# Kernel optimization log

Hardware: AMD Instinct MI355X
Metric: run time of the kernel (lower is better)

The kernel has to match this reference:

```python
import jax, jax.numpy as jnp
import numpy as np

LAMBDA_ENERGY = 0.1   # CONFIG['lambda_energy']
EPS = 1e-6            # CONFIG['eps']
TEMP = 1.0


def setup_inputs() -> dict:
    key = jax.random.key(0)
    k0, k1, k2, k3, k4 = jax.random.split(key, 5)
    B, S, D, N = 8, 4096, 512, 1024
    z_real = jax.random.normal(k0, (B, S, D), dtype=jnp.float32)
    z_imag = jax.random.normal(k1, (B, S, D), dtype=jnp.float32)
    # prev symbol distribution: a proper simplex distribution over symbols
    prev_sym_dist = jax.nn.softmax(jax.random.normal(k2, (B, S, N), dtype=jnp.float32), axis=-1)
    codebook = jax.random.normal(k3, (N, 2 * D), dtype=jnp.float32) * 0.2
    adjacency_energy = jax.random.normal(k4, (N, N), dtype=jnp.float32)
    return {"z_real": z_real, "z_imag": z_imag, "prev_sym_dist": prev_sym_dist,
            "codebook": codebook, "adjacency_energy": adjacency_energy}


def reference(z_real, z_imag, prev_sym_dist, codebook, adjacency_energy):
    D = z_real.shape[-1]
    z_flat = jnp.concatenate([z_real, z_imag], axis=-1)  # [B,S,2D]

    # squared-distance to codebook entries, normalized by feature dim
    d_content = (jnp.sum(z_flat * z_flat, axis=-1, keepdims=True)
                 + jnp.sum(codebook * codebook, axis=-1)
                 - 2.0 * jnp.einsum('bsd,nd->bsn', z_flat, codebook)) / z_flat.shape[-1]

    # ComplexityModulator (eval mode): running_var buffer == 1.0
    mag = jnp.sqrt(z_real * z_real + z_imag * z_imag)  # |z|
    batch_var = jnp.var(mag, ddof=1)                   # torch .var() is unbiased
    modulation = jax.nn.softplus(batch_var / (1.0 + EPS))

    # graph-bias gating
    graph_bias = jnp.einsum('bsn,nm->bsm', prev_sym_dist, adjacency_energy)
    d_total = d_content - (LAMBDA_ENERGY * modulation) * jax.nn.sigmoid(graph_bias)

    # eval path: soft_one_hot = softmax(logits / temp)
    probs = jax.nn.softmax(-d_total / TEMP, axis=-1)   # [B,S,N]
    z_q_flat = jnp.einsum('bsn,nd->bsd', probs, codebook)  # [B,S,2D]

    energy = jnp.mean(d_total)
    return z_q_flat[..., :D], z_q_flat[..., D:], energy
```

## Files before the change

### kernel.cpp

```cpp
#include <hip/hip_runtime.h>

typedef float    floatx4 __attribute__((ext_vector_type(4)));
typedef short    short8  __attribute__((ext_vector_type(8)));
typedef _Float16 h4      __attribute__((ext_vector_type(4)));

#define NROWS 32768
#define KD    1024
#define DD    512

__device__ __forceinline__ unsigned pk_bf16(unsigned hi_bits, unsigned lo_bits) {
    return __builtin_amdgcn_perm(hi_bits, lo_bits, 0x07060302u);
}

__device__ __forceinline__ void gload_lds16(const void* g, void* l) {
    __builtin_amdgcn_global_load_lds((__attribute__((address_space(1))) void*)(void*)g,
                                     (__attribute__((address_space(3))) void*)l,
                                     16, 0, 0);
}

__global__ void k_row(const float* __restrict__ zr, const float* __restrict__ zi,
                      unsigned short* __restrict__ zb,
                      float* __restrict__ zz, float* __restrict__ mgp) {
    int r = blockIdx.x, t = threadIdx.x;
    const float2* a2 = (const float2*)(zr + (size_t)r * DD);
    const float2* b2 = (const float2*)(zi + (size_t)r * DD);
    float2 a = a2[t], b = b2[t];
    unsigned* zrow = (unsigned*)(zb + (size_t)r * KD);
    zrow[t]       = pk_bf16(__float_as_uint(a.y), __float_as_uint(a.x));
    zrow[256 + t] = pk_bf16(__float_as_uint(b.y), __float_as_uint(b.x));
    float m0 = a.x * a.x + b.x * b.x;
    float m1 = a.y * a.y + b.y * b.y;
    float sm2 = m0 + m1;
    float smg = sqrtf(m0) + sqrtf(m1);
    for (int o = 32; o > 0; o >>= 1) { sm2 += __shfl_down(sm2, o); smg += __shfl_down(smg, o); }
    __shared__ float r2[4], rg[4];
    int wv = t >> 6, ln = t & 63;
    if (ln == 0) { r2[wv] = sm2; rg[wv] = smg; }
    __syncthreads();
    if (t == 0) {
        zz[r]  = r2[0] + r2[1] + r2[2] + r2[3];
        mgp[r] = rg[0] + rg[1] + rg[2] + rg[3];
    }
}

__global__ void k_prev(const float* __restrict__ p, unsigned short* __restrict__ pb) {
    size_t i = ((size_t)blockIdx.x * 256 + threadIdx.x) * 8;
    const uint4* g = (const uint4*)(p + i);
    uint4 u0 = g[0], u1 = g[1];
    uint4 o;
    o.x = pk_bf16(u0.y, u0.x); o.y = pk_bf16(u0.w, u0.z);
    o.z = pk_bf16(u1.y, u1.x); o.w = pk_bf16(u1.w, u1.z);
    *(uint4*)(pb + i) = o;
}

__global__ void k_cb(const float* __restrict__ cb, unsigned short* __restrict__ cb_bf,
                     float* __restrict__ cc) {
    int n = blockIdx.x, t = threadIdx.x;
    const float4* src = (const float4*)(cb + (size_t)n * KD);
    float4 v = src[t];
    float s = v.x * v.x + v.y * v.y + v.z * v.z + v.w * v.w;
    unsigned d0 = pk_bf16(__float_as_uint(v.y), __float_as_uint(v.x));
    unsigned d1 = pk_bf16(__float_as_uint(v.w), __float_as_uint(v.z));
    *(uint2*)(cb_bf + (size_t)n * KD + t * 4) = make_uint2(d0, d1);
    for (int o = 32; o > 0; o >>= 1) s += __shfl_down(s, o);
    __shared__ float rd[4];
    int wv = t >> 6, ln = t & 63;
    if (ln == 0) rd[wv] = s;
    __syncthreads();
    if (t == 0) cc[n] = rd[0] + rd[1] + rd[2] + rd[3];
}

__global__ void k_tr(const float* __restrict__ src, unsigned short* __restrict__ dst) {
    __shared__ float tile[32][33];
    int bx = blockIdx.x * 32, by = blockIdx.y * 32;
    int tx = threadIdx.x, ty = threadIdx.y;
    for (int r = ty; r < 32; r += 8)
        tile[r][tx] = src[(size_t)(by + r) * 1024 + bx + tx];
    __syncthreads();
    for (int r = ty; r < 32; r += 8)
        dst[(size_t)(bx + r) * 1024 + by + tx] =
            (unsigned short)(__float_as_uint(tile[tx][r]) >> 16);
}

__global__ void k_scalar(const float* __restrict__ zz, const float* __restrict__ mgp,
                         double* __restrict__ sums, float* __restrict__ lam) {
    int t = threadIdx.x;
    double s2 = 0.0, sg = 0.0;
    for (int i = t; i < NROWS; i += 1024) { s2 += (double)zz[i]; sg += (double)mgp[i]; }
    __shared__ double l2[1024], lg[1024];
    l2[t] = s2; lg[t] = sg; __syncthreads();
    for (int s = 512; s > 0; s >>= 1) {
        if (t < s) { l2[t] += l2[t + s]; lg[t] += lg[t + s]; }
        __syncthreads();
    }
    if (t == 0) {
        double M = 16777216.0;
        double var = (l2[0] - lg[0] * lg[0] / M) / (M - 1.0);
        double x = var / (1.0 + 1e-6);
        double mod = log1p(exp(x));
        lam[0] = (float)(0.1 * mod);
        sums[1] = l2[0];
    }
}

__global__ __launch_bounds__(512, 4)
void k_gemm12(const unsigned short* __restrict__ zb,
              const unsigned short* __restrict__ pb,
              const unsigned short* __restrict__ cb_bf,
              const unsigned short* __restrict__ adjT_bf,
              const float* __restrict__ cc, const float* __restrict__ lam_p,
              _Float16* __restrict__ s_out, double* __restrict__ e_acc) {
    __shared__ unsigned short A1[128 * 32], A2[128 * 32], B1[128 * 32], B2[128 * 32];
    int tid = threadIdx.x, bid = blockIdx.x;
    int rt = bid >> 3, ct = bid & 7;
    int row0 = rt * 128, col0 = ct * 128;
    int wv = tid >> 6, ln = tid & 63;
    int wr = (wv >> 1) * 32;
    int wc = (wv & 1) * 64;

    floatx4 acc1[2][4], acc2[2][4];
    for (int i = 0; i < 2; ++i)
        for (int j = 0; j < 4; ++j) {
            floatx4 z4 = {0.f, 0.f, 0.f, 0.f};
            acc1[i][j] = z4; acc2[i][j] = z4;
        }

    int rr = tid >> 2, k8 = (tid & 3) << 3;
    unsigned short* lA1 = &A1[(wv * 64) * 8];
    unsigned short* lA2 = &A2[(wv * 64) * 8];
    unsigned short* lB1 = &B1[(wv * 64) * 8];
    unsigned short* lB2 = &B2[(wv * 64) * 8];

    for (int kb = 0; kb < KD; kb += 32) {
        gload_lds16(zb      + (size_t)(row0 + rr) * KD + kb + k8, lA1);
        gload_lds16(pb      + (size_t)(row0 + rr) * KD + kb + k8, lA2);
        gload_lds16(cb_bf   + (size_t)(col0 + rr) * KD + kb + k8, lB1);
        gload_lds16(adjT_bf + (size_t)(col0 + rr) * KD + kb + k8, lB2);
        __syncthreads();

        short8 af[2], bfr[4];
        for (int i = 0; i < 2; ++i)
            af[i] = *(const short8*)&A1[(wr + i * 16 + (ln & 15)) * 32 + (ln >> 4) * 8];
        for (int j = 0; j < 4; ++j)
            bfr[j] = *(const short8*)&B1[(wc + j * 16 + (ln & 15)) * 32 + (ln >> 4) * 8];
        for (int mi = 0; mi < 2; ++mi)
            for (int ni = 0; ni < 4; ++ni)
                acc1[mi][ni] = __builtin_amdgcn_mfma_f32_16x16x32_bf16(af[mi], bfr[ni], acc1[mi][ni], 0, 0, 0);
        for (int i = 0; i < 2; ++i)
            af[i] = *(const short8*)&A2[(wr + i * 16 + (ln & 15)) * 32 + (ln >> 4) * 8];
        for (int j = 0; j < 4; ++j)
            bfr[j] = *(const short8*)&B2[(wc + j * 16 + (ln & 15)) * 32 + (ln >> 4) * 8];
        for (int mi = 0; mi < 2; ++mi)
            for (int ni = 0; ni < 4; ++ni)
                acc2[mi][ni] = __builtin_amdgcn_mfma_f32_16x16x32_bf16(af[mi], bfr[ni], acc2[mi][ni], 0, 0, 0);
        __syncthreads();
    }

    float lam = *lam_p;
    float esum = 0.f;
    for (int mi = 0; mi < 2; ++mi) {
        int rbase = row0 + wr + mi * 16 + (ln >> 4) * 4;
        for (int ni = 0; ni < 4; ++ni) {
            int col = col0 + wc + ni * 16 + (ln & 15);
            float ccol = cc[col];
            for (int r2 = 0; r2 < 4; ++r2) {
                float d1 = acc1[mi][ni][r2];
                float d2 = acc2[mi][ni][r2];
                float sv = (ccol - 2.f * d1) * (1.0f / 1024.0f) - lam / (1.f + __expf(-d2));
                esum += sv;
                s_out[(size_t)(rbase + r2) * KD + col] = (_Float16)sv;
            }
        }
    }
    for (int o = 32; o > 0; o >>= 1) esum += __shfl_down(esum, o);
    if (ln == 0) atomicAdd(e_acc, (double)esum);
}

__global__ void k_softmax(_Float16* __restrict__ sp) {
    int row = blockIdx.x, t = threadIdx.x;
    int wv = t >> 6, ln = t & 63;
    _Float16* srow = sp + (size_t)row * KD;
    h4 v = *(const h4*)(srow + t * 4);
    float x0 = -(float)v.x, x1 = -(float)v.y, x2 = -(float)v.z, x3 = -(float)v.w;
    float mx = fmaxf(fmaxf(x0, x1), fmaxf(x2, x3));
    for (int o = 1; o < 64; o <<= 1) mx = fmaxf(mx, __shfl_xor(mx, o));
    __shared__ float redm[4];
    if (ln == 0) redm[wv] = mx;
    __syncthreads();
    mx = fmaxf(fmaxf(redm[0], redm[1]), fmaxf(redm[2], redm[3]));
    float e0 = __expf(x0 - mx), e1 = __expf(x1 - mx), e2 = __expf(x2 - mx), e3 = __expf(x3 - mx);
    float ss = e0 + e1 + e2 + e3;
    for (int o = 1; o < 64; o <<= 1) ss += __shfl_xor(ss, o);
    __shared__ float reds[4];
    if (ln == 0) reds[wv] = ss;
    __syncthreads();
    ss = reds[0] + reds[1] + reds[2] + reds[3];
    float inv = 1.f / ss;
    unsigned p0 = __float_as_uint(e0 * inv), p1 = __float_as_uint(e1 * inv);
    unsigned p2 = __float_as_uint(e2 * inv), p3 = __float_as_uint(e3 * inv);
    *(uint2*)((unsigned short*)srow + t * 4) = make_uint2(pk_bf16(p1, p0), pk_bf16(p3, p2));
}

__global__ __launch_bounds__(512, 4)
void k_gemm3(const unsigned short* __restrict__ probs,
             const unsigned short* __restrict__ cbT_bf,
             float* __restrict__ outR, float* __restrict__ outI) {
    __shared__ unsigned short At[128 * 32], Bt[128 * 32];
    int tid = threadIdx.x, bid = blockIdx.x;
    int rt = bid >> 3, ct = bid & 7;
    int row0 = rt * 128, col0 = ct * 128;
    int wv = tid >> 6, ln = tid & 63;
    int wr = (wv >> 1) * 32;
    int wc = (wv & 1) * 64;

    floatx4 acc[2][4];
    for (int i = 0; i < 2; ++i)
        for (int j = 0; j < 4; ++j) { floatx4 z4 = {0.f, 0.f, 0.f, 0.f}; acc[i][j] = z4; }

    int rr = tid >> 2, k8 = (tid & 3) << 3;
    unsigned short* lA = &At[(wv * 64) * 8];
    unsigned short* lB = &Bt[(wv * 64) * 8];

    for (int kb = 0; kb < KD; kb += 32) {
        gload_lds16(probs  + (size_t)(row0 + rr) * KD + kb + k8, lA);
        gload_lds16(cbT_bf + (size_t)(col0 + rr) * KD + kb + k8, lB);
        __syncthreads();
        short8 af[2], bfr[4];
        for (int i = 0; i < 2; ++i)
            af[i] = *(const short8*)&At[(wr + i * 16 + (ln & 15)) * 32 + (ln >> 4) * 8];
        for (int j = 0; j < 4; ++j)
            bfr[j] = *(const short8*)&Bt[(wc + j * 16 + (ln & 15)) * 32 + (ln >> 4) * 8];
        for (int mi = 0; mi < 2; ++mi)
            for (int ni = 0; ni < 4; ++ni)
                acc[mi][ni] = __builtin_amdgcn_mfma_f32_16x16x32_bf16(af[mi], bfr[ni], acc[mi][ni], 0, 0, 0);
        __syncthreads();
    }

    for (int mi = 0; mi < 2; ++mi) {
        int rbase = row0 + wr + mi * 16 + (ln >> 4) * 4;
        for (int ni = 0; ni < 4; ++ni) {
            int col = col0 + wc + ni * 16 + (ln & 15);
            for (int r2 = 0; r2 < 4; ++r2) {
                float v = acc[mi][ni][r2];
                size_t row = (size_t)(rbase + r2);
                if (col < DD) outR[row * DD + col] = v;
                else          outI[row * DD + (col - DD)] = v;
            }
        }
    }
}

__global__ void k_final(const double* __restrict__ sums, float* __restrict__ outE) {
    outE[0] = (float)((sums[0] + sums[1]) / 33554432.0);
}

extern "C" void kernel_launch(void* const* d_in, const int* in_sizes, int n_in,
                              void* d_out, int out_size, void* d_ws, size_t ws_size,
                              hipStream_t stream) {
    const float* zr   = (const float*)d_in[0];
    const float* zi   = (const float*)d_in[1];
    const float* prev = (const float*)d_in[2];
    const float* cb   = (const float*)d_in[3];
    const float* adj  = (const float*)d_in[4];
    float* out  = (float*)d_out;
    float* outR = out;
    float* outI = out + (size_t)16777216;
    float* outE = out + (size_t)33554432;

    unsigned short* zb = (unsigned short*)d_out;
    unsigned short* pb = (unsigned short*)d_out + (size_t)33554432;

    char* ws = (char*)d_ws;
    double* sums          = (double*)ws;
    float*  lam           = (float*)(ws + 16);
    float*  zz            = (float*)(ws + 256);
    float*  mgp           = (float*)(ws + 131328);
    float*  cc            = (float*)(ws + 262400);
    unsigned short* cb_bf = (unsigned short*)(ws + 266496);
    unsigned short* adjT  = (unsigned short*)(ws + 2363648);
    unsigned short* cbT   = (unsigned short*)(ws + 4460800);
    _Float16*       sbuf  = (_Float16*)(ws + 6557952);

    hipMemsetAsync(d_ws, 0, 32, stream);
    k_row<<<32768, 256, 0, stream>>>(zr, zi, zb, zz, mgp);
    k_prev<<<16384, 256, 0, stream>>>(prev, pb);
    k_cb<<<1024, 256, 0, stream>>>(cb, cb_bf, cc);
    k_tr<<<dim3(32, 32), dim3(32, 8), 0, stream>>>(adj, adjT);
    k_tr<<<dim3(32, 32), dim3(32, 8), 0, stream>>>(cb, cbT);
    k_scalar<<<1, 1024, 0, stream>>>(zz, mgp, sums, lam);
    k_gemm12<<<2048, 512, 0, stream>>>(zb, pb, cb_bf, adjT, cc, lam, sbuf, sums);
    k_softmax<<<32768, 256, 0, stream>>>(sbuf);
    k_gemm3<<<2048, 512, 0, stream>>>((const unsigned short*)sbuf, cbT, outR, outI);
    k_final<<<1, 1, 0, stream>>>(sums, outE);
}
```

Measured before the change: 766.7 us.

## Deepen GEMM K-tile to 64 with XOR-swizzled LDS and grid remap

Both MFMA GEMM kernels now stage a K-chunk of 64 instead of 32 per barrier pair, which halves the number of __syncthreads round-trips. The global-to-LDS copies place 16-byte segments at XOR-swizzled positions (segment ^ row&7) to cut LDS bank conflicts on the fragment reads. The block index is also remapped so that consecutive blocks take different row tiles of the same column tile, changing L2 reuse of the B operand. LDS use doubles per block, which may lower occupancy for the four-buffer kernel.

```diff
diff --git a/kernel.cpp b/kernel.cpp
--- a/kernel.cpp
+++ b/kernel.cpp
@@ -110,9 +110,10 @@
               const unsigned short* __restrict__ adjT_bf,
               const float* __restrict__ cc, const float* __restrict__ lam_p,
               _Float16* __restrict__ s_out, double* __restrict__ e_acc) {
-    __shared__ unsigned short A1[128 * 32], A2[128 * 32], B1[128 * 32], B2[128 * 32];
+    __shared__ unsigned short A1[128 * 64], A2[128 * 64], B1[128 * 64], B2[128 * 64];
     int tid = threadIdx.x, bid = blockIdx.x;
-    int rt = bid >> 3, ct = bid & 7;
+    int wg = (bid & 7) * 256 + (bid >> 3);
+    int rt = wg >> 3, ct = wg & 7;
     int row0 = rt * 128, col0 = ct * 128;
     int wv = tid >> 6, ln = tid & 63;
     int wr = (wv >> 1) * 32;
@@ -125,34 +126,61 @@
             acc1[i][j] = z4; acc2[i][j] = z4;
         }
 
-    int rr = tid >> 2, k8 = (tid & 3) << 3;
-    unsigned short* lA1 = &A1[(wv * 64) * 8];
-    unsigned short* lA2 = &A2[(wv * 64) * 8];
-    unsigned short* lB1 = &B1[(wv * 64) * 8];
-    unsigned short* lB2 = &B2[(wv * 64) * 8];
-
-    for (int kb = 0; kb < KD; kb += 32) {
-        gload_lds16(zb      + (size_t)(row0 + rr) * KD + kb + k8, lA1);
-        gload_lds16(pb      + (size_t)(row0 + rr) * KD + kb + k8, lA2);
-        gload_lds16(cb_bf   + (size_t)(col0 + rr) * KD + kb + k8, lB1);
-        gload_lds16(adjT_bf + (size_t)(col0 + rr) * KD + kb + k8, lB2);
-        __syncthreads();
-
-        short8 af[2], bfr[4];
-        for (int i = 0; i < 2; ++i)
-            af[i] = *(const short8*)&A1[(wr + i * 16 + (ln & 15)) * 32 + (ln >> 4) * 8];
-        for (int j = 0; j < 4; ++j)
-            bfr[j] = *(const short8*)&B1[(wc + j * 16 + (ln & 15)) * 32 + (ln >> 4) * 8];
-        for (int mi = 0; mi < 2; ++mi)
-            for (int ni = 0; ni < 4; ++ni)
-                acc1[mi][ni] = __builtin_amdgcn_mfma_f32_16x16x32_bf16(af[mi], bfr[ni], acc1[mi][ni], 0, 0, 0);
-        for (int i = 0; i < 2; ++i)
-            af[i] = *(const short8*)&A2[(wr + i * 16 + (ln & 15)) * 32 + (ln >> 4) * 8];
-        for (int j = 0; j < 4; ++j)
-            bfr[j] = *(const short8*)&B2[(wc + j * 16 + (ln & 15)) * 32 + (ln >> 4) * 8];
-        for (int mi = 0; mi < 2; ++mi)
-            for (int ni = 0; ni < 4; ++ni)
-                acc2[mi][ni] = __builtin_amdgcn_mfma_f32_16x16x32_bf16(af[mi], bfr[ni], acc2[mi][ni], 0, 0, 0);
+    int r0 = tid >> 3,         s0 = tid & 7;
+    int r1 = (512 + tid) >> 3;
+    size_t aoff0 = (size_t)(row0 + r0) * KD + ((s0 ^ (r0 & 7)) << 3);
+    size_t aoff1 = (size_t)(row0 + r1) * KD + ((s0 ^ (r1 & 7)) << 3);
+    size_t boff0 = (size_t)(col0 + r0) * KD + ((s0 ^ (r0 & 7)) << 3);
+    size_t boff1 = (size_t)(col0 + r1) * KD + ((s0 ^ (r1 & 7)) << 3);
+    int l0 = wv * 512;
+    int l1 = 4096 + wv * 512;
+
+    for (int kb = 0; kb < KD; kb += 64) {
+        gload_lds16(zb      + aoff0 + kb, &A1[l0]);
+        gload_lds16(zb      + aoff1 + kb, &A1[l1]);
+        gload_lds16(pb      + aoff0 + kb, &A2[l0]);
+        gload_lds16(pb      + aoff1 + kb, &A2[l1]);
+        gload_lds16(cb_bf   + boff0 + kb, &B1[l0]);
+        gload_lds16(cb_bf   + boff1 + kb, &B1[l1]);
+        gload_lds16(adjT_bf + boff0 + kb, &B2[l0]);
+        gload_lds16(adjT_bf + boff1 + kb, &B2[l1]);
+        __syncthreads();
+
+        #pragma unroll
+        for (int kk = 0; kk < 2; ++kk) {
+            int sb = kk * 4 + (ln >> 4);
+            short8 af[2], bfr[4];
+            #pragma unroll
+            for (int i = 0; i < 2; ++i) {
+                int r = wr + i * 16 + (ln & 15);
+                af[i] = *(const short8*)&A1[r * 64 + ((sb ^ (r & 7)) << 3)];
+            }
+            #pragma unroll
+            for (int j = 0; j < 4; ++j) {
+                int r = wc + j * 16 + (ln & 15);
+                bfr[j] = *(const short8*)&B1[r * 64 + ((sb ^ (r & 7)) << 3)];
+            }
+            #pragma unroll
+            for (int mi = 0; mi < 2; ++mi)
+                #pragma unroll
+                for (int ni = 0; ni < 4; ++ni)
+                    acc1[mi][ni] = __builtin_amdgcn_mfma_f32_16x16x32_bf16(af[mi], bfr[ni], acc1[mi][ni], 0, 0, 0);
+            #pragma unroll
+            for (int i = 0; i < 2; ++i) {
+                int r = wr + i * 16 + (ln & 15);
+                af[i] = *(const short8*)&A2[r * 64 + ((sb ^ (r & 7)) << 3)];
+            }
+            #pragma unroll
+            for (int j = 0; j < 4; ++j) {
+                int r = wc + j * 16 + (ln & 15);
+                bfr[j] = *(const short8*)&B2[r * 64 + ((sb ^ (r & 7)) << 3)];
+            }
+            #pragma unroll
+            for (int mi = 0; mi < 2; ++mi)
+                #pragma unroll
+                for (int ni = 0; ni < 4; ++ni)
+                    acc2[mi][ni] = __builtin_amdgcn_mfma_f32_16x16x32_bf16(af[mi], bfr[ni], acc2[mi][ni], 0, 0, 0);
+        }
         __syncthreads();
     }
 
@@ -205,9 +233,10 @@
 void k_gemm3(const unsigned short* __restrict__ probs,
              const unsigned short* __restrict__ cbT_bf,
              float* __restrict__ outR, float* __restrict__ outI) {
-    __shared__ unsigned short At[128 * 32], Bt[128 * 32];
+    __shared__ unsigned short At[128 * 64], Bt[128 * 64];
     int tid = threadIdx.x, bid = blockIdx.x;
-    int rt = bid >> 3, ct = bid & 7;
+    int wg = (bid & 7) * 256 + (bid >> 3);
+    int rt = wg >> 3, ct = wg & 7;
     int row0 = rt * 128, col0 = ct * 128;
     int wv = tid >> 6, ln = tid & 63;
     int wr = (wv >> 1) * 32;
@@ -217,22 +246,42 @@
     for (int i = 0; i < 2; ++i)
         for (int j = 0; j < 4; ++j) { floatx4 z4 = {0.f, 0.f, 0.f, 0.f}; acc[i][j] = z4; }
 
-    int rr = tid >> 2, k8 = (tid & 3) << 3;
-    unsigned short* lA = &At[(wv * 64) * 8];
-    unsigned short* lB = &Bt[(wv * 64) * 8];
-
-    for (int kb = 0; kb < KD; kb += 32) {
-        gload_lds16(probs  + (size_t)(row0 + rr) * KD + kb + k8, lA);
-        gload_lds16(cbT_bf + (size_t)(col0 + rr) * KD + kb + k8, lB);
-        __syncthreads();
-        short8 af[2], bfr[4];
-        for (int i = 0; i < 2; ++i)
-            af[i] = *(const short8*)&At[(wr + i * 16 + (ln & 15)) * 32 + (ln >> 4) * 8];
-        for (int j = 0; j < 4; ++j)
-            bfr[j] = *(const short8*)&Bt[(wc + j * 16 + (ln & 15)) * 32 + (ln >> 4) * 8];
-        for (int mi = 0; mi < 2; ++mi)
-            for (int ni = 0; ni < 4; ++ni)
-                acc[mi][ni] = __builtin_amdgcn_mfma_f32_16x16x32_bf16(af[mi], bfr[ni], acc[mi][ni], 0, 0, 0);
+    int r0 = tid >> 3,         s0 = tid & 7;
+    int r1 = (512 + tid) >> 3;
+    size_t aoff0 = (size_t)(row0 + r0) * KD + ((s0 ^ (r0 & 7)) << 3);
+    size_t aoff1 = (size_t)(row0 + r1) * KD + ((s0 ^ (r1 & 7)) << 3);
+    size_t boff0 = (size_t)(col0 + r0) * KD + ((s0 ^ (r0 & 7)) << 3);
+    size_t boff1 = (size_t)(col0 + r1) * KD + ((s0 ^ (r1 & 7)) << 3);
+    int l0 = wv * 512;
+    int l1 = 4096 + wv * 512;
+
+    for (int kb = 0; kb < KD; kb += 64) {
+        gload_lds16(probs  + aoff0 + kb, &At[l0]);
+        gload_lds16(probs  + aoff1 + kb, &At[l1]);
+        gload_lds16(cbT_bf + boff0 + kb, &Bt[l0]);
+        gload_lds16(cbT_bf + boff1 + kb, &Bt[l1]);
+        __syncthreads();
+
+        #pragma unroll
+        for (int kk = 0; kk < 2; ++kk) {
+            int sb = kk * 4 + (ln >> 4);
+            short8 af[2], bfr[4];
+            #pragma unroll
+            for (int i = 0; i < 2; ++i) {
+                int r = wr + i * 16 + (ln & 15);
+                af[i] = *(const short8*)&At[r * 64 + ((sb ^ (r & 7)) << 3)];
+            }
+            #pragma unroll
+            for (int j = 0; j < 4; ++j) {
+                int r = wc + j * 16 + (ln & 15);
+                bfr[j] = *(const short8*)&Bt[r * 64 + ((sb ^ (r & 7)) << 3)];
+            }
+            #pragma unroll
+            for (int mi = 0; mi < 2; ++mi)
+                #pragma unroll
+                for (int ni = 0; ni < 4; ++ni)
+                    acc[mi][ni] = __builtin_amdgcn_mfma_f32_16x16x32_bf16(af[mi], bfr[ni], acc[mi][ni], 0, 0, 0);
+        }
         __syncthreads();
     }
 
```

After: 698.4 us. 8.9% less time.
